# Kernel optimization log

Hardware: AMD Instinct MI355X
Metric: run time of the kernel (lower is better)

## Reference

```python
import jax, jax.numpy as jnp
import numpy as np

B, H, SQ, SK, D = 2, 16, 2048, 2048, 128
INV_SCALE = 0.05  # scores are DIVIDED by this (i.e., multiplied by 20)


def setup_inputs() -> dict:
    k0 = jax.random.key(0)
    kq, kk, kv, km = jax.random.split(k0, 4)
    query = jax.random.normal(kq, (B, H, SQ, D), dtype=jnp.float32)
    key = jax.random.normal(kk, (B, H, SK, D), dtype=jnp.float32)
    value = jax.random.normal(kv, (B, H, SK, D), dtype=jnp.float32)
    padding_mask = jax.random.randint(km, (D,), 0, 2).astype(jnp.bool_)
    input_mask = jnp.zeros((D,), dtype=jnp.bool_)  # unused by forward, kept for signature parity
    return {"query": query, "key": key, "value": value,
            "padding_mask": padding_mask, "input_mask": input_mask}


def reference(query, key, value, padding_mask, input_mask):
    # scores: [B, H, SQ, SK]
    qk = jnp.einsum('bhqd,bhkd->bhqk', query, key)
    attn = jax.nn.softmax(qk / INV_SCALE, axis=-1)
    # dropout with undefined dropout_p in source; eval mode -> identity
    out = jnp.einsum('bhqk,bhkd->bhqd', attn, value)  # [B, H, SQ, D]
    # masked_fill over the LAST (head) dim, per padding_mask[None,None,None,:]
    out = jnp.where(padding_mask[None, None, None, :], jnp.float32(0.0), out)
    return out
```

## Files before the change

### kernel.cpp

```cpp
#include <hip/hip_runtime.h>
#include <math.h>

#define SQ_ 2048
#define SK_ 2048
#define D_  128
#define BH_ 32
#define SCALE_L2E 28.853900817779268f
#define TAU 13.0f

typedef _Float16 f16;
typedef __attribute__((ext_vector_type(8))) f16    f16x8;
typedef __attribute__((ext_vector_type(4))) f16    f16x4;
typedef __attribute__((ext_vector_type(4))) float  floatx4;
typedef __attribute__((ext_vector_type(8))) __bf16 bf16x8;
typedef __attribute__((ext_vector_type(4))) __bf16 bf16x4;
typedef __attribute__((ext_vector_type(2))) __bf16 bf16x2;

#define TILE_ELEMS 24576
#define WS_NEED ((size_t)BH_ * 32 * TILE_ELEMS * 2)

typedef __attribute__((address_space(3))) unsigned int lds_uint;
typedef const __attribute__((address_space(1))) unsigned int glob_uint;
__device__ __forceinline__ void async16(const void* g, void* l) {
    __builtin_amdgcn_global_load_lds((glob_uint*)g, (lds_uint*)l, 16, 0, 0);
}

__global__ void prep(const float* __restrict__ K, const float* __restrict__ V,
                     f16* __restrict__ ws)
{
    __shared__ float sB[64 * 132];
    const int id = blockIdx.x;
    const int t  = threadIdx.x;
    const size_t src_off = ((size_t)(id >> 5) * SK_ + (id & 31) * 64) * D_;
    f16* tile = ws + (size_t)id * TILE_ELEMS;

    const float* srcK = K + src_off;
#pragma unroll
    for (int i = 0; i < 8; ++i) {
        const int idx = t + i * 256, row = idx >> 5, c4 = (idx & 31) * 4;
        *(floatx4*)&sB[row * 132 + c4] = *(const floatx4*)(srcK + row * 128 + c4);
    }
    __syncthreads();
#pragma unroll
    for (int h = 0; h < 4; ++h) {
        const int g = t + h * 256, key = g & 63, c4q = g >> 6;
        floatx4 a = *(const floatx4*)&sB[key * 132 + c4q * 8];
        floatx4 b = *(const floatx4*)&sB[key * 132 + c4q * 8 + 4];
        f16x8 hi, lo;
#pragma unroll
        for (int j = 0; j < 4; ++j) {
            f16 x = (f16)a[j]; hi[j] = x; lo[j] = (f16)(a[j] - (float)x);
        }
#pragma unroll
        for (int j = 0; j < 4; ++j) {
            f16 x = (f16)b[j]; hi[4 + j] = x; lo[4 + j] = (f16)(b[j] - (float)x);
        }
        *(f16x8*)(tile + g * 8) = hi;
        *(f16x8*)(tile + 8192 + g * 8) = lo;
    }
    __syncthreads();
    const float* srcV = V + src_off;
#pragma unroll
    for (int i = 0; i < 8; ++i) {
        const int idx = t + i * 256, row = idx >> 5, c4 = (idx & 31) * 4;
        *(floatx4*)&sB[row * 132 + c4] = *(const floatx4*)(srcV + row * 128 + c4);
    }
    __syncthreads();
#pragma unroll
    for (int h = 0; h < 4; ++h) {
        const int g = t + h * 256, kq = g >> 7, d = g & 127;
        f16x8 p;
#pragma unroll
        for (int e = 0; e < 8; ++e) p[e] = (f16)sB[(kq * 8 + e) * 132 + d];
        *(f16x8*)(tile + 16384 + g * 8) = p;
    }
}

__global__ __launch_bounds__(256, 2)
void fattn4(const float* __restrict__ Q, const f16* __restrict__ ws,
            const int* __restrict__ mask, float* __restrict__ Out)
{
    __shared__ __align__(16) f16 sT[TILE_ELEMS];

    const int tid  = threadIdx.x;
    const int w    = tid >> 6;
    const int lane = tid & 63;
    const int m    = lane & 15;
    const int quad = lane >> 4;
    const int id   = blockIdx.x;
    const int bh   = (id & 7) * 4 + ((id >> 3) & 3);
    const int qt   = id >> 5;

    f16x8 qhi[2][4], qlo[2][4];
#pragma unroll
    for (int rt = 0; rt < 2; ++rt) {
        const int qrow = qt * 128 + w * 32 + rt * 16 + m;
        const float* qp = Q + ((size_t)(bh * SQ_ + qrow)) * D_;
#pragma unroll
        for (int c = 0; c < 4; ++c) {
            floatx4 a = *(const floatx4*)(qp + c * 32 + quad * 8);
            floatx4 b = *(const floatx4*)(qp + c * 32 + quad * 8 + 4);
#pragma unroll
            for (int j = 0; j < 4; ++j) {
                float x = a[j] * SCALE_L2E;
                f16 h = (f16)x;
                qhi[rt][c][j] = h; qlo[rt][c][j] = (f16)(x - (float)h);
            }
#pragma unroll
            for (int j = 0; j < 4; ++j) {
                float x = b[j] * SCALE_L2E;
                f16 h = (f16)x;
                qhi[rt][c][4 + j] = h; qlo[rt][c][4 + j] = (f16)(x - (float)h);
            }
        }
    }

    f16x4 ones4;
#pragma unroll
    for (int j = 0; j < 4; ++j) ones4[j] = (f16)1.0f;

    floatx4 O[2][8], lac[2];
    float mf[2] = {-INFINITY, -INFINITY};
#pragma unroll
    for (int rt = 0; rt < 2; ++rt) {
        lac[rt] = (floatx4){0.f, 0.f, 0.f, 0.f};
#pragma unroll
        for (int t = 0; t < 8; ++t) O[rt][t] = (floatx4){0.f, 0.f, 0.f, 0.f};
    }

    const f16* wsB = ws + (size_t)bh * 32 * TILE_ELEMS;

#pragma unroll
    for (int j = 0; j < 8; ++j)
        async16(wsB + (w * 8 + j) * 512 + lane * 8, &sT[(w * 8 + j) * 512]);
#pragma unroll
    for (int j = 0; j < 4; ++j)
        async16(wsB + 16384 + (w * 4 + j) * 512 + lane * 8, &sT[16384 + (w * 4 + j) * 512]);
    __syncthreads();

    for (int kt = 0; kt < 32; ++kt) {
        floatx4 S[2][4];
#pragma unroll
        for (int rt = 0; rt < 2; ++rt)
#pragma unroll
            for (int nt = 0; nt < 4; ++nt) S[rt][nt] = (floatx4){0.f, 0.f, 0.f, 0.f};
#pragma unroll
        for (int c = 0; c < 4; ++c) {
#pragma unroll
            for (int nt = 0; nt < 4; ++nt) {
                const int g = (c * 4 + quad) * 64 + nt * 16 + m;
                f16x8 kh = *(const f16x8*)&sT[g * 8];
                f16x8 kl = *(const f16x8*)&sT[8192 + g * 8];
#pragma unroll
                for (int rt = 0; rt < 2; ++rt) {
                    S[rt][nt] = __builtin_amdgcn_mfma_f32_16x16x32_f16(kh, qhi[rt][c], S[rt][nt], 0, 0, 0);
                    S[rt][nt] = __builtin_amdgcn_mfma_f32_16x16x32_f16(kl, qhi[rt][c], S[rt][nt], 0, 0, 0);
                    S[rt][nt] = __builtin_amdgcn_mfma_f32_16x16x32_f16(kh, qlo[rt][c], S[rt][nt], 0, 0, 0);
                }
            }
        }

        __syncthreads();
        if (kt + 1 < 32) {
            const f16* nk = wsB + (size_t)(kt + 1) * TILE_ELEMS;
#pragma unroll
            for (int j = 0; j < 8; ++j)
                async16(nk + (w * 8 + j) * 512 + lane * 8, &sT[(w * 8 + j) * 512]);
        }

        float mx[2];
#pragma unroll
        for (int rt = 0; rt < 2; ++rt) {
            float v0 = fmaxf(fmaxf(S[rt][0][0], S[rt][0][1]), fmaxf(S[rt][0][2], S[rt][0][3]));
            float v1 = fmaxf(fmaxf(S[rt][1][0], S[rt][1][1]), fmaxf(S[rt][1][2], S[rt][1][3]));
            float v2 = fmaxf(fmaxf(S[rt][2][0], S[rt][2][1]), fmaxf(S[rt][2][2], S[rt][2][3]));
            float v3 = fmaxf(fmaxf(S[rt][3][0], S[rt][3][1]), fmaxf(S[rt][3][2], S[rt][3][3]));
            float v = fmaxf(fmaxf(v0, v1), fmaxf(v2, v3));
            v = fmaxf(v, __shfl_xor(v, 16));
            v = fmaxf(v, __shfl_xor(v, 32));
            mx[rt] = v;
        }
        const bool upd = (mx[0] > mf[0] + TAU) || (mx[1] > mf[1] + TAU);
        if (__ballot(upd)) {
#pragma unroll
            for (int rt = 0; rt < 2; ++rt) {
                const float mn = fmaxf(mf[rt], mx[rt]);
                const float al = exp2f(mf[rt] - mn);
                mf[rt] = mn;
                lac[rt][0] *= al;
#pragma unroll
                for (int t = 0; t < 8; ++t)
#pragma unroll
                    for (int r = 0; r < 4; ++r) O[rt][t][r] *= al;
            }
        }

        f16x4 P[2][4];
#pragma unroll
        for (int rt = 0; rt < 2; ++rt)
#pragma unroll
            for (int nt = 0; nt < 4; ++nt)
#pragma unroll
                for (int r = 0; r < 4; ++r)
                    P[rt][nt][r] = (f16)exp2f(S[rt][nt][r] - mf[rt]);

#pragma unroll
        for (int rt = 0; rt < 2; ++rt)
#pragma unroll
            for (int nt = 0; nt < 4; ++nt)
                lac[rt] = __builtin_amdgcn_mfma_f32_16x16x16f16(ones4, P[rt][nt], lac[rt], 0, 0, 0);

#pragma unroll
        for (int t = 0; t < 8; ++t) {
#pragma unroll
            for (int nt = 0; nt < 4; ++nt) {
                f16x4 vf = *(const f16x4*)&sT[16384 +
                    ((nt * 2 + (quad >> 1)) * 128 + t * 16 + m) * 8 + (quad & 1) * 4];
                O[0][t] = __builtin_amdgcn_mfma_f32_16x16x16f16(vf, P[0][nt], O[0][t], 0, 0, 0);
                O[1][t] = __builtin_amdgcn_mfma_f32_16x16x16f16(vf, P[1][nt], O[1][t], 0, 0, 0);
            }
        }

        __syncthreads();
        if (kt + 1 < 32) {
            const f16* nv = wsB + (size_t)(kt + 1) * TILE_ELEMS + 16384;
#pragma unroll
            for (int j = 0; j < 4; ++j)
                async16(nv + (w * 4 + j) * 512 + lane * 8, &sT[16384 + (w * 4 + j) * 512]);
        }
    }

#pragma unroll
    for (int rt = 0; rt < 2; ++rt) {
        const float inv = 1.0f / lac[rt][0];
        const int qrow = qt * 128 + w * 32 + rt * 16 + m;
        float* outp = Out + ((size_t)(bh * SQ_ + qrow)) * D_;
#pragma unroll
        for (int t = 0; t < 8; ++t) {
            const int d0 = t * 16 + quad * 4;
            floatx4 o;
#pragma unroll
            for (int r = 0; r < 4; ++r) {
                const float mk = (mask[d0 + r] != 0) ? 0.0f : 1.0f;
                o[r] = O[rt][t][r] * inv * mk;
            }
            *(floatx4*)(outp + d0) = o;
        }
    }
}

#define KSTR 136
#define VSTR 40
#define PSTR 40
__global__ __launch_bounds__(256, 2)
void fattn_kernel(const float* __restrict__ Q, const float* __restrict__ K,
                  const float* __restrict__ V, const int* __restrict__ mask,
                  float* __restrict__ Out)
{
    __shared__ __align__(16) __bf16 sKhi[32 * KSTR];
    __shared__ __align__(16) __bf16 sKlo[32 * KSTR];
    __shared__ __align__(16) __bf16 sVt[128 * VSTR];
    __shared__ __align__(16) __bf16 sP2[4 * 16 * PSTR];

    const int tid  = threadIdx.x;
    const int w    = tid >> 6;
    const int lane = tid & 63;
    const int m    = lane & 15;
    const int quad = lane >> 4;
    const int qt   = blockIdx.x;
    const int bh   = blockIdx.y;

    bf16x8 qhi[4], qlo[4];
    {
        const int qrow = qt * 64 + w * 16 + m;
        const float* qp = Q + ((size_t)(bh * SQ_ + qrow)) * D_;
#pragma unroll
        for (int c = 0; c < 4; ++c) {
            const int d0 = c * 32 + quad * 8;
            floatx4 a = *(const floatx4*)(qp + d0);
            floatx4 b = *(const floatx4*)(qp + d0 + 4);
#pragma unroll
            for (int j = 0; j < 4; ++j) {
                float x = a[j] * 20.0f;
                __bf16 h = (__bf16)x;
                qhi[c][j] = h; qlo[c][j] = (__bf16)(x - (float)h);
            }
#pragma unroll
            for (int j = 0; j < 4; ++j) {
                float x = b[j] * 20.0f;
                __bf16 h = (__bf16)x;
                qhi[c][4 + j] = h; qlo[c][4 + j] = (__bf16)(x - (float)h);
            }
        }
    }

    floatx4 O[8];
#pragma unroll
    for (int t = 0; t < 8; ++t) O[t] = (floatx4){0.f, 0.f, 0.f, 0.f};
    float m_i[4] = {-INFINITY, -INFINITY, -INFINITY, -INFINITY};
    float l_i[4] = {0.f, 0.f, 0.f, 0.f};

    const float* Kbh = K + (size_t)bh * SK_ * D_;
    const float* Vbh = V + (size_t)bh * SK_ * D_;
    __bf16* sPw = sP2 + w * 16 * PSTR;

    for (int kt = 0; kt < SK_ / 32; ++kt) {
        const int kbase = kt * 32;
#pragma unroll
        for (int i = 0; i < 4; ++i) {
            const int lin = i * 1024 + tid * 4;
            const int key = lin >> 7;
            const int d   = lin & 127;
            floatx4 v = *(const floatx4*)(Kbh + (kbase + key) * D_ + d);
            bf16x4 h4, l4;
#pragma unroll
            for (int j = 0; j < 4; ++j) {
                __bf16 h = (__bf16)v[j]; h4[j] = h; l4[j] = (__bf16)(v[j] - (float)h);
            }
            *(bf16x4*)&sKhi[key * KSTR + d] = h4;
            *(bf16x4*)&sKlo[key * KSTR + d] = l4;
        }
#pragma unroll
        for (int i = 0; i < 2; ++i) {
            const int pi   = i * 256 + tid;
            const int kp   = (pi & 15) * 2;
            const int dblk = (pi >> 4);
            const int d0   = dblk * 4;
            floatx4 v0 = *(const floatx4*)(Vbh + (kbase + kp) * D_ + d0);
            floatx4 v1 = *(const floatx4*)(Vbh + (kbase + kp + 1) * D_ + d0);
#pragma unroll
            for (int j = 0; j < 4; ++j) {
                bf16x2 p2; p2[0] = (__bf16)v0[j]; p2[1] = (__bf16)v1[j];
                *(bf16x2*)&sVt[(d0 + j) * VSTR + kp] = p2;
            }
        }
        __syncthreads();

        floatx4 Sv[2];
#pragma unroll
        for (int nt = 0; nt < 2; ++nt) {
            floatx4 acc = (floatx4){0.f, 0.f, 0.f, 0.f};
#pragma unroll
            for (int c = 0; c < 4; ++c) {
                const int off = (nt * 16 + m) * KSTR + c * 32 + quad * 8;
                bf16x8 kh = *(const bf16x8*)&sKhi[off];
                bf16x8 kl = *(const bf16x8*)&sKlo[off];
                acc = __builtin_amdgcn_mfma_f32_16x16x32_bf16(qhi[c], kh, acc, 0, 0, 0);
                acc = __builtin_amdgcn_mfma_f32_16x16x32_bf16(qlo[c], kh, acc, 0, 0, 0);
                acc = __builtin_amdgcn_mfma_f32_16x16x32_bf16(qhi[c], kl, acc, 0, 0, 0);
            }
            Sv[nt] = acc;
        }

        float alpha[4];
#pragma unroll
        for (int r = 0; r < 4; ++r) {
            float tmax = fmaxf(Sv[0][r], Sv[1][r]);
#pragma unroll
            for (int off = 1; off < 16; off <<= 1)
                tmax = fmaxf(tmax, __shfl_xor(tmax, off, 64));
            const float mn = fmaxf(m_i[r], tmax);
            const float a  = __expf(m_i[r] - mn);
            const float p0 = __expf(Sv[0][r] - mn);
            const float p1 = __expf(Sv[1][r] - mn);
            Sv[0][r] = p0; Sv[1][r] = p1;
            float rs = p0 + p1;
#pragma unroll
            for (int off = 1; off < 16; off <<= 1)
                rs += __shfl_xor(rs, off, 64);
            l_i[r] = l_i[r] * a + rs;
            m_i[r] = mn;
            alpha[r] = a;
        }
#pragma unroll
        for (int t = 0; t < 8; ++t)
#pragma unroll
            for (int r = 0; r < 4; ++r)
                O[t][r] *= alpha[r];

#pragma unroll
        for (int r = 0; r < 4; ++r) {
            sPw[(quad * 4 + r) * PSTR + m]      = (__bf16)Sv[0][r];
            sPw[(quad * 4 + r) * PSTR + 16 + m] = (__bf16)Sv[1][r];
        }
        __asm__ volatile("s_waitcnt lgkmcnt(0)" ::: "memory");
        bf16x8 pf = *(const bf16x8*)&sPw[m * PSTR + quad * 8];

#pragma unroll
        for (int t = 0; t < 8; ++t) {
            bf16x8 vf = *(const bf16x8*)&sVt[(t * 16 + m) * VSTR + quad * 8];
            O[t] = __builtin_amdgcn_mfma_f32_16x16x32_bf16(pf, vf, O[t], 0, 0, 0);
        }
        __syncthreads();
    }

    float inv[4];
#pragma unroll
    for (int r = 0; r < 4; ++r) inv[r] = 1.0f / l_i[r];
    const int qrow0 = qt * 64 + w * 16 + quad * 4;
    float* outp = Out + ((size_t)(bh * SQ_ + qrow0)) * D_;
#pragma unroll
    for (int t = 0; t < 8; ++t) {
        const int d = t * 16 + m;
        const float mk = (mask[d] != 0) ? 0.0f : 1.0f;
#pragma unroll
        for (int r = 0; r < 4; ++r)
            outp[r * D_ + d] = O[t][r] * inv[r] * mk;
    }
}

extern "C" void kernel_launch(void* const* d_in, const int* in_sizes, int n_in,
                              void* d_out, int out_size, void* d_ws, size_t ws_size,
                              hipStream_t stream) {
    const float* Q = (const float*)d_in[0];
    const float* K = (const float*)d_in[1];
    const float* V = (const float*)d_in[2];
    const int* mask = (const int*)d_in[3];
    float* out = (float*)d_out;

    if (ws_size >= WS_NEED) {
        f16* ws = (f16*)d_ws;
        prep<<<1024, 256, 0, stream>>>(K, V, ws);
        fattn4<<<512, 256, 0, stream>>>(Q, ws, mask, out);
    } else {
        dim3 grid(SQ_ / 64, BH_);
        fattn_kernel<<<grid, 256, 0, stream>>>(Q, K, V, mask, out);
    }
}
```

Before: 276.0 us.

## Overlap softmax exp with QK MFMAs and swizzle V tile to avoid bank conflicts

Splits the QK^T score computation into two halves so a partial max over the first half is taken, then the exponentials for the first half are computed against the running max while the second half's MFMAs execute, interleaving VALU exp work with matrix work. If the full max later triggers a rescale, the first-half P values are recomputed. Separately, the prep kernel swizzles the V half-blocks by column group, and the attention kernel reads with a matching XOR offset to reduce LDS bank conflicts. The initial running max changes from -inf to -1e5, which avoids NaNs from exp2 on the speculative first pass. The cost is extra code complexity and occasional recomputation of the exponentials.

```diff
diff --git a/kernel.cpp b/kernel.cpp
--- a/kernel.cpp
+++ b/kernel.cpp
@@ -69,15 +69,16 @@
 #pragma unroll
     for (int h = 0; h < 4; ++h) {
         const int g = t + h * 256, kq = g >> 7, d = g & 127;
+        const int swz = ((d >> 3) & 1) * 4;
         f16x8 p;
 #pragma unroll
-        for (int e = 0; e < 8; ++e) p[e] = (f16)sB[(kq * 8 + e) * 132 + d];
+        for (int e = 0; e < 8; ++e) p[e] = (f16)sB[(kq * 8 + (e ^ swz)) * 132 + d];
         *(f16x8*)(tile + 16384 + g * 8) = p;
     }
 }
 
 __global__ __launch_bounds__(256, 2)
-void fattn4(const float* __restrict__ Q, const f16* __restrict__ ws,
+void fattn5(const float* __restrict__ Q, const f16* __restrict__ ws,
             const int* __restrict__ mask, float* __restrict__ Out)
 {
     __shared__ __align__(16) f16 sT[TILE_ELEMS];
@@ -120,7 +121,7 @@
     for (int j = 0; j < 4; ++j) ones4[j] = (f16)1.0f;
 
     floatx4 O[2][8], lac[2];
-    float mf[2] = {-INFINITY, -INFINITY};
+    float mf[2] = {-1e5f, -1e5f};
 #pragma unroll
     for (int rt = 0; rt < 2; ++rt) {
         lac[rt] = (floatx4){0.f, 0.f, 0.f, 0.f};
@@ -129,6 +130,7 @@
     }
 
     const f16* wsB = ws + (size_t)bh * 32 * TILE_ELEMS;
+    const int vhalf = ((quad & 1) ^ ((m >> 3) & 1)) * 4;
 
 #pragma unroll
     for (int j = 0; j < 8; ++j)
@@ -144,10 +146,11 @@
         for (int rt = 0; rt < 2; ++rt)
 #pragma unroll
             for (int nt = 0; nt < 4; ++nt) S[rt][nt] = (floatx4){0.f, 0.f, 0.f, 0.f};
+
 #pragma unroll
         for (int c = 0; c < 4; ++c) {
 #pragma unroll
-            for (int nt = 0; nt < 4; ++nt) {
+            for (int nt = 0; nt < 2; ++nt) {
                 const int g = (c * 4 + quad) * 64 + nt * 16 + m;
                 f16x8 kh = *(const f16x8*)&sT[g * 8];
                 f16x8 kl = *(const f16x8*)&sT[8192 + g * 8];
@@ -160,6 +163,51 @@
             }
         }
 
+        float mxA[2];
+#pragma unroll
+        for (int rt = 0; rt < 2; ++rt) {
+            float v0 = fmaxf(fmaxf(S[rt][0][0], S[rt][0][1]), fmaxf(S[rt][0][2], S[rt][0][3]));
+            float v1 = fmaxf(fmaxf(S[rt][1][0], S[rt][1][1]), fmaxf(S[rt][1][2], S[rt][1][3]));
+            float v = fmaxf(v0, v1);
+            v = fmaxf(v, __shfl_xor(v, 16));
+            v = fmaxf(v, __shfl_xor(v, 32));
+            mxA[rt] = v;
+        }
+
+        f16x4 P[2][4];
+#pragma unroll
+        for (int c = 0; c < 4; ++c) {
+#pragma unroll
+            for (int nt = 2; nt < 4; ++nt) {
+                const int g = (c * 4 + quad) * 64 + nt * 16 + m;
+                f16x8 kh = *(const f16x8*)&sT[g * 8];
+                f16x8 kl = *(const f16x8*)&sT[8192 + g * 8];
+#pragma unroll
+                for (int rt = 0; rt < 2; ++rt) {
+                    S[rt][nt] = __builtin_amdgcn_mfma_f32_16x16x32_f16(kh, qhi[rt][c], S[rt][nt], 0, 0, 0);
+                    S[rt][nt] = __builtin_amdgcn_mfma_f32_16x16x32_f16(kl, qhi[rt][c], S[rt][nt], 0, 0, 0);
+                    S[rt][nt] = __builtin_amdgcn_mfma_f32_16x16x32_f16(kh, qlo[rt][c], S[rt][nt], 0, 0, 0);
+                }
+            }
+            {
+                const int rt = c >> 1, sn = c & 1;
+#pragma unroll
+                for (int r = 0; r < 4; ++r)
+                    P[rt][sn][r] = (f16)exp2f(S[rt][sn][r] - mf[rt]);
+            }
+        }
+
+        float mx[2];
+#pragma unroll
+        for (int rt = 0; rt < 2; ++rt) {
+            float v2 = fmaxf(fmaxf(S[rt][2][0], S[rt][2][1]), fmaxf(S[rt][2][2], S[rt][2][3]));
+            float v3 = fmaxf(fmaxf(S[rt][3][0], S[rt][3][1]), fmaxf(S[rt][3][2], S[rt][3][3]));
+            float v = fmaxf(v2, v3);
+            v = fmaxf(v, __shfl_xor(v, 16));
+            v = fmaxf(v, __shfl_xor(v, 32));
+            mx[rt] = fmaxf(mxA[rt], v);
+        }
+
         __syncthreads();
         if (kt + 1 < 32) {
             const f16* nk = wsB + (size_t)(kt + 1) * TILE_ELEMS;
@@ -168,18 +216,6 @@
                 async16(nk + (w * 8 + j) * 512 + lane * 8, &sT[(w * 8 + j) * 512]);
         }
 
-        float mx[2];
-#pragma unroll
-        for (int rt = 0; rt < 2; ++rt) {
-            float v0 = fmaxf(fmaxf(S[rt][0][0], S[rt][0][1]), fmaxf(S[rt][0][2], S[rt][0][3]));
-            float v1 = fmaxf(fmaxf(S[rt][1][0], S[rt][1][1]), fmaxf(S[rt][1][2], S[rt][1][3]));
-            float v2 = fmaxf(fmaxf(S[rt][2][0], S[rt][2][1]), fmaxf(S[rt][2][2], S[rt][2][3]));
-            float v3 = fmaxf(fmaxf(S[rt][3][0], S[rt][3][1]), fmaxf(S[rt][3][2], S[rt][3][3]));
-            float v = fmaxf(fmaxf(v0, v1), fmaxf(v2, v3));
-            v = fmaxf(v, __shfl_xor(v, 16));
-            v = fmaxf(v, __shfl_xor(v, 32));
-            mx[rt] = v;
-        }
         const bool upd = (mx[0] > mf[0] + TAU) || (mx[1] > mf[1] + TAU);
         if (__ballot(upd)) {
 #pragma unroll
@@ -192,14 +228,17 @@
                 for (int t = 0; t < 8; ++t)
 #pragma unroll
                     for (int r = 0; r < 4; ++r) O[rt][t][r] *= al;
-            }
-        }
-
-        f16x4 P[2][4];
+#pragma unroll
+                for (int sn = 0; sn < 2; ++sn)
+#pragma unroll
+                    for (int r = 0; r < 4; ++r)
+                        P[rt][sn][r] = (f16)exp2f(S[rt][sn][r] - mf[rt]);
+            }
+        }
 #pragma unroll
         for (int rt = 0; rt < 2; ++rt)
 #pragma unroll
-            for (int nt = 0; nt < 4; ++nt)
+            for (int nt = 2; nt < 4; ++nt)
 #pragma unroll
                 for (int r = 0; r < 4; ++r)
                     P[rt][nt][r] = (f16)exp2f(S[rt][nt][r] - mf[rt]);
@@ -215,7 +254,7 @@
 #pragma unroll
             for (int nt = 0; nt < 4; ++nt) {
                 f16x4 vf = *(const f16x4*)&sT[16384 +
-                    ((nt * 2 + (quad >> 1)) * 128 + t * 16 + m) * 8 + (quad & 1) * 4];
+                    ((nt * 2 + (quad >> 1)) * 128 + t * 16 + m) * 8 + vhalf];
                 O[0][t] = __builtin_amdgcn_mfma_f32_16x16x16f16(vf, P[0][nt], O[0][t], 0, 0, 0);
                 O[1][t] = __builtin_amdgcn_mfma_f32_16x16x16f16(vf, P[1][nt], O[1][t], 0, 0, 0);
             }
@@ -421,7 +460,7 @@
     if (ws_size >= WS_NEED) {
         f16* ws = (f16*)d_ws;
         prep<<<1024, 256, 0, stream>>>(K, V, ws);
-        fattn4<<<512, 256, 0, stream>>>(Q, ws, mask, out);
+        fattn5<<<512, 256, 0, stream>>>(Q, ws, mask, out);
     } else {
         dim3 grid(SQ_ / 64, BH_);
         fattn_kernel<<<grid, 256, 0, stream>>>(Q, K, V, mask, out);
```

Measured after the change: 283.7 us. +2.8%, slower.
